# Kernel optimization log

Hardware: AMD Instinct MI355X
Metric: run time of the kernel (lower is better)

## Reference

```python
import jax, jax.numpy as jnp
import numpy as np

B, T, C, H = 64, 256, 384, 6
HS = C // H  # 64
EPS = 1e-3  # keras LayerNormalization default epsilon


def layernorm(x, gamma, beta):
    mu = jnp.mean(x, axis=-1, keepdims=True)
    var = jnp.var(x, axis=-1, keepdims=True)
    return (x - mu) * jax.lax.rsqrt(var + EPS) * gamma + beta


def setup_inputs() -> dict:
    key = jax.random.key(0)
    ks = jax.random.split(key, 12)
    s = lambda fan_in: 1.0 / np.sqrt(fan_in)
    return {
        "x": jax.random.normal(ks[0], (B, T, C), dtype=jnp.float32),
        "Wq": jax.random.normal(ks[1], (H, C, HS), dtype=jnp.float32) * s(C),
        "Wk": jax.random.normal(ks[2], (H, C, HS), dtype=jnp.float32) * s(C),
        "Wv": jax.random.normal(ks[3], (H, C, HS), dtype=jnp.float32) * s(C),
        "Wp": jax.random.normal(ks[4], (C, C), dtype=jnp.float32) * s(C),
        "bp": jnp.zeros((C,), dtype=jnp.float32),
        "W1": jax.random.normal(ks[5], (C, 4 * C), dtype=jnp.float32) * s(C),
        "b1": jnp.zeros((4 * C,), dtype=jnp.float32),
        "W2": jax.random.normal(ks[6], (4 * C, C), dtype=jnp.float32) * s(4 * C),
        "b2": jnp.zeros((C,), dtype=jnp.float32),
        "g1": jnp.ones((C,), dtype=jnp.float32),
        "be1": jnp.zeros((C,), dtype=jnp.float32),
        "g2": jnp.ones((C,), dtype=jnp.float32),
        "be2": jnp.zeros((C,), dtype=jnp.float32),
    }


def reference(x, Wq, Wk, Wv, Wp, bp, W1, b1, W2, b2, g1, be1, g2, be2):
    # --- self-attention sub-block (dropout is identity at inference) ---
    h = layernorm(x, g1, be1)                              # [B,T,C]
    q = jnp.einsum('btc,hcd->bhtd', h, Wq)                 # [B,H,T,HS]
    k = jnp.einsum('btc,hcd->bhtd', h, Wk)
    v = jnp.einsum('btc,hcd->bhtd', h, Wv)
    scale = HS ** -0.5
    wei = jnp.einsum('bhtd,bhsd->bhts', q, k) * scale      # [B,H,T,T]
    causal = jnp.tril(jnp.ones((T, T), dtype=bool))
    wei = jnp.where(causal[None, None], wei, -jnp.inf)
    att = jax.nn.softmax(wei, axis=-1)
    o = jnp.einsum('bhts,bhsd->bthd', att, v).reshape(B, T, C)  # concat heads
    sa = o @ Wp + bp
    x = x + sa
    # --- feed-forward sub-block ---
    h2 = layernorm(x, g2, be2)
    ff = jax.nn.relu(h2 @ W1 + b1) @ W2 + b2
    return x + ff
```

## Files before the change

### kernel.cpp

```cpp
#include <hip/hip_runtime.h>
#include <hip/hip_bf16.h>
#include <math.h>

#define Bn 64
#define Tn 256
#define Cn 384
#define Hn 6
#define HSn 64
#define FFn 1536
#define EPSn 1e-3f
#define SECn 6291456

typedef __attribute__((ext_vector_type(4))) float f32x4;
typedef __attribute__((ext_vector_type(2))) float f32x2;
typedef __attribute__((ext_vector_type(8))) short short8;
typedef __attribute__((ext_vector_type(4))) short short4v;
typedef __attribute__((ext_vector_type(2))) short short2v;

__device__ __forceinline__ short f2bf(float v) {
    __hip_bfloat16 h = __float2bfloat16(v);
    return *(short*)&h;
}


__global__ __launch_bounds__(256) void ln_pack_kernel(const float* __restrict__ x,
                                                      const float* __restrict__ g,
                                                      const float* __restrict__ be,
                                                      __hip_bfloat16* __restrict__ outPk) {
    int mt = blockIdx.x;
    int tid = threadIdx.x;
    int lane = tid & 63, wave = tid >> 6;
    __shared__ short rows[16 * 392];
#pragma unroll
    for (int i = 0; i < 4; i++) {
        int r = wave * 4 + i;
        const float* xr = x + ((size_t)mt * 16 + r) * Cn;
        f32x4 a = *(const f32x4*)(xr + lane * 4);
        f32x2 b = *(const f32x2*)(xr + 256 + lane * 2);
        float s = a.x + a.y + a.z + a.w + b.x + b.y;
#pragma unroll
        for (int off = 32; off; off >>= 1) s += __shfl_xor(s, off);
        float mu = s * (1.0f / Cn);
        f32x4 da = a - mu;
        f32x2 db = b - mu;
        float sq = da.x * da.x + da.y * da.y + da.z * da.z + da.w * da.w + db.x * db.x + db.y * db.y;
#pragma unroll
        for (int off = 32; off; off >>= 1) sq += __shfl_xor(sq, off);
        float rs = rsqrtf(sq * (1.0f / Cn) + EPSn);
        f32x4 g4 = *(const f32x4*)(g + lane * 4);
        f32x2 g2 = *(const f32x2*)(g + 256 + lane * 2);
        f32x4 e4 = *(const f32x4*)(be + lane * 4);
        f32x2 e2 = *(const f32x2*)(be + 256 + lane * 2);
        f32x4 y4 = da * rs * g4 + e4;
        f32x2 y2 = db * rs * g2 + e2;
        short4v o4 = {f2bf(y4.x), f2bf(y4.y), f2bf(y4.z), f2bf(y4.w)};
        *(short4v*)(&rows[r * 392 + lane * 4]) = o4;
        short2v o2 = {f2bf(y2.x), f2bf(y2.y)};
        *(short2v*)(&rows[r * 392 + 256 + lane * 2]) = o2;
    }
    __syncthreads();
    int r = lane & 15, q = lane >> 4;
#pragma unroll
    for (int p = 0; p < 3; p++) {
        int f = p * 4 + (tid >> 6);
        short8 v = *(const short8*)(&rows[r * 392 + f * 32 + q * 8]);
        *(short8*)((short*)outPk + ((size_t)mt * 12 + f) * 512 + lane * 8) = v;
    }
}

__global__ __launch_bounds__(256) void pack_b_kernel(const float* __restrict__ W,
                                                     __hip_bfloat16* __restrict__ out,
                                                     int K, int N) {
    int id = blockIdx.x * 256 + threadIdx.x;
    if (id >= K * N) return;
    int tile = id >> 9, lane = (id >> 3) & 63, j = id & 7;
    int ntiles = N >> 4;
    int k = (tile / ntiles) * 32 + ((lane >> 4) << 3) + j;
    int n = (tile % ntiles) * 16 + (lane & 15);
    out[id] = __float2bfloat16(W[(size_t)k * N + n]);
}

__global__ __launch_bounds__(256) void pack_qkv_kernel(const float* __restrict__ Wq,
                                                       const float* __restrict__ Wk,
                                                       const float* __restrict__ Wv,
                                                       __hip_bfloat16* __restrict__ out) {
    int id = blockIdx.x * 256 + threadIdx.x;
    if (id >= Cn * 1152) return;
    int tile = id >> 9, lane = (id >> 3) & 63, j = id & 7;
    int k = (tile / 72) * 32 + ((lane >> 4) << 3) + j;
    int n = (tile % 72) * 16 + (lane & 15);
    int sec = n / Cn, rem = n % Cn;
    int hh = rem >> 6, d = rem & 63;
    const float* W = (sec == 0) ? Wq : ((sec == 1) ? Wk : Wv);
    out[id] = __float2bfloat16(W[((size_t)hh * Cn + k) * HSn + d]);
}

template <int KK, int NN, int EPI>
__global__ __launch_bounds__(256) void gemm_mfma(const __hip_bfloat16* __restrict__ Apk,
                                                 const __hip_bfloat16* __restrict__ Bp,
                                                 const float* __restrict__ bias,
                                                 const float* __restrict__ resid,
                                                 float* __restrict__ outF,
                                                 __hip_bfloat16* __restrict__ outB) {
    constexpr int GX = NN / 64;
    constexpr int K32 = KK / 32;
    constexpr int NT16 = NN / 16;
    __shared__ __align__(16) char lds_raw[4 * 4864];

    int l = blockIdx.x;
    int xcd = l & 7, i = l >> 3;
    int rowblk = xcd * 16 + i / GX;
    int colblk = i - (i / GX) * GX;

    int lane = threadIdx.x & 63, wave = threadIdx.x >> 6;
    int lrow = lane & 15, lquad = lane >> 4;
    int m0 = rowblk * 128;
    int n0 = colblk * 64;
    int mt0 = (m0 >> 4) + wave * 2;

    f32x4 acc[2][4];
#pragma unroll
    for (int st = 0; st < 2; st++)
#pragma unroll
        for (int nt = 0; nt < 4; nt++) acc[st][nt] = (f32x4){0.f, 0.f, 0.f, 0.f};

    const short* a0p = (const short*)Apk + ((size_t)mt0 * K32) * 512 + lane * 8;
    const short* a1p = a0p + (size_t)K32 * 512;
    const short* bp0 = (const short*)Bp + ((size_t)(n0 >> 4)) * 512 + lane * 8;

#pragma unroll 6
    for (int kc = 0; kc < K32; kc++) {
        short8 af0 = *(const short8*)(a0p + (size_t)kc * 512);
        short8 af1 = *(const short8*)(a1p + (size_t)kc * 512);
#pragma unroll
        for (int nt = 0; nt < 4; nt++) {
            short8 bf = *(const short8*)(bp0 + ((size_t)kc * NT16 + nt) * 512);
            acc[0][nt] = __builtin_amdgcn_mfma_f32_16x16x32_bf16(af0, bf, acc[0][nt], 0, 0, 0);
            acc[1][nt] = __builtin_amdgcn_mfma_f32_16x16x32_bf16(af1, bf, acc[1][nt], 0, 0, 0);
        }
    }

    if (EPI == 1) {
        float* twf = (float*)(lds_raw + wave * 4864);
        float bnv[4];
#pragma unroll
        for (int nt = 0; nt < 4; nt++) bnv[nt] = bias[n0 + nt * 16 + lrow];
#pragma unroll
        for (int st = 0; st < 2; st++) {
            int mbase = m0 + (2 * wave + st) * 16;
#pragma unroll
            for (int nt = 0; nt < 4; nt++)
#pragma unroll
                for (int r = 0; r < 4; r++)
                    twf[(lquad * 4 + r) * 76 + nt * 16 + lrow] = acc[st][nt][r] + bnv[nt];
            int row = lane >> 2, seg = lane & 3;
            int m = mbase + row;
            const float* rrow = resid + (size_t)m * NN + n0 + seg * 16;
            float* orow = outF + (size_t)m * NN + n0 + seg * 16;
#pragma unroll
            for (int c = 0; c < 4; c++) {
                f32x4 vv = *(const f32x4*)(&twf[row * 76 + seg * 16 + c * 4]);
                f32x4 rv = *(const f32x4*)(rrow + c * 4);
                *(f32x4*)(orow + c * 4) = vv + rv;
            }
            __builtin_amdgcn_s_waitcnt(0);
        }
    } else {
        short* tws = (short*)(lds_raw + wave * 4864);
        float bnv[4];
        if (EPI == 2) {
#pragma unroll
            for (int nt = 0; nt < 4; nt++) bnv[nt] = bias[n0 + nt * 16 + lrow];
        }
#pragma unroll
        for (int st = 0; st < 2; st++)
#pragma unroll
            for (int nt = 0; nt < 4; nt++)
#pragma unroll
                for (int r = 0; r < 4; r++) {
                    float v = acc[st][nt][r];
                    if (EPI == 2) v = fmaxf(v + bnv[nt], 0.0f);
                    tws[(st * 16 + lquad * 4 + r) * 72 + nt * 16 + lrow] = f2bf(v);
                }
        if (EPI == 2) {
#pragma unroll
            for (int st2 = 0; st2 < 2; st2++) {
                int mt = (m0 >> 4) + wave * 2 + st2;
#pragma unroll
                for (int kcl = 0; kcl < 2; kcl++) {
                    int kc = (n0 >> 5) + kcl;
                    short8 v = *(const short8*)(
                        &tws[(st2 * 16 + (lane & 15)) * 72 + kcl * 32 + (lane >> 4) * 8]);
                    *(short8*)((short*)outB + ((size_t)mt * (NN / 32) + kc) * 512 + lane * 8) = v;
                }
            }
        } else {
            int sec = n0 / 384;
            int rem0 = n0 - sec * 384;
            int hh = rem0 >> 6;
            int b = m0 >> 8;
            int t_base = (m0 & 255) + wave * 32;
            int bh2 = b * Hn + hh;
            if (sec < 2) {
                short* outp = (short*)outB + (size_t)sec * SECn + (size_t)bh2 * 16384 +
                              (size_t)(t_base >> 4) * 1024 + lane * 8;
#pragma unroll
                for (int st2 = 0; st2 < 2; st2++)
#pragma unroll
                    for (int kc = 0; kc < 2; kc++) {
                        short8 v8 = *(const short8*)(
                            &tws[(st2 * 16 + (lane & 15)) * 72 + kc * 32 + (lane >> 4) * 8]);
                        *(short8*)(outp + (st2 * 2 + kc) * 512) = v8;
                    }
            } else {
                short* vout = (short*)outB + (size_t)2 * SECn + (size_t)bh2 * 16384 +
                              (size_t)((t_base >> 5) * 4) * 512;
#pragma unroll
                for (int dt = 0; dt < 4; dt++) {
                    short8 v8;
#pragma unroll
                    for (int j = 0; j < 8; j++) {
                        int t_loc = ((lane >> 4) << 3) + j;
                        v8[j] = tws[t_loc * 72 + dt * 16 + (lane & 15)];
                    }
                    *(short8*)(vout + dt * 512 + lane * 8) = v8;
                }
            }
        }
    }
}

__global__ __launch_bounds__(256) void attn_mfma_kernel(const __hip_bfloat16* __restrict__ qp,
                                                        const __hip_bfloat16* __restrict__ kp,
                                                        const __hip_bfloat16* __restrict__ vp,
                                                        __hip_bfloat16* __restrict__ o) {
    __shared__ short Pl[4 * 4096];
    int blk = blockIdx.x;
    int bh = blk % (Bn * Hn);
    int jg = blk / (Bn * Hn);
    int b = bh / Hn, hh = bh - b * Hn;
    int tid = threadIdx.x;
    int lane = tid & 63, wave = tid >> 6;
    int c16 = lane & 15, quad = lane >> 4;
    int qt = (wave << 2) + ((wave & 1) ? (3 - jg) : jg);

    const short* qs = (const short*)qp + (size_t)bh * 16384 + (size_t)qt * 1024 + lane * 8;
    const short* ks = (const short*)kp + (size_t)bh * 16384 + lane * 8;
    const short* vs = (const short*)vp + (size_t)bh * 16384 + lane * 8;
    short* Pw = Pl + wave * 4096;

    short8 aq0 = *(const short8*)(qs);
    short8 aq1 = *(const short8*)(qs + 512);

    int st_max = qt;
    int kb_count = (qt + 2) >> 1;
    int covered = kb_count * 2;
    int qrow0 = qt * 16;

    f32x4 accS[16];
#pragma unroll
    for (int st = 0; st < 16; st++) accS[st] = (f32x4){0.f, 0.f, 0.f, 0.f};
#pragma unroll
    for (int st = 0; st < 16; st++) {
        if (st <= st_max) {
            short8 bk0 = *(const short8*)(ks + st * 1024);
            short8 bk1 = *(const short8*)(ks + st * 1024 + 512);
            accS[st] = __builtin_amdgcn_mfma_f32_16x16x32_bf16(aq0, bk0, accS[st], 0, 0, 0);
            accS[st] = __builtin_amdgcn_mfma_f32_16x16x32_bf16(aq1, bk1, accS[st], 0, 0, 0);
        }
    }

    float inv[4];
#pragma unroll
    for (int r = 0; r < 4; r++) {
        int row = qrow0 + quad * 4 + r;
        float mx = -INFINITY;
#pragma unroll
        for (int st = 0; st < 16; st++) {
            if (st <= st_max) {
                int col = st * 16 + c16;
                float a = (col <= row) ? accS[st][r] * 0.125f : -INFINITY;
                accS[st][r] = a;
                mx = fmaxf(mx, a);
            }
        }
#pragma unroll
        for (int off = 8; off; off >>= 1) mx = fmaxf(mx, __shfl_xor(mx, off));
        float sum = 0.f;
#pragma unroll
        for (int st = 0; st < 16; st++) {
            if (st < covered) {
                float e = 0.0f;
                if (st <= st_max) {
                    e = __expf(accS[st][r] - mx);
                    sum += e;
                }
                int c = st * 16 + c16;
                Pw[(c >> 5) * 512 + (((c >> 3) & 3) * 16 + quad * 4 + r) * 8 + (c & 7)] =
                    f2bf(e);
            }
        }
#pragma unroll
        for (int off = 8; off; off >>= 1) sum += __shfl_xor(sum, off);
        inv[r] = 1.0f / sum;
    }

    f32x4 accO[4];
#pragma unroll
    for (int nt = 0; nt < 4; nt++) accO[nt] = (f32x4){0.f, 0.f, 0.f, 0.f};
#pragma unroll
    for (int kbi = 0; kbi < 8; kbi++) {
        if (kbi < kb_count) {
            short8 ap = *(const short8*)(Pw + kbi * 512 + lane * 8);
#pragma unroll
            for (int nt = 0; nt < 4; nt++) {
                short8 bv = *(const short8*)(vs + (kbi * 4 + nt) * 512);
                accO[nt] = __builtin_amdgcn_mfma_f32_16x16x32_bf16(ap, bv, accO[nt], 0, 0, 0);
            }
        }
    }

#pragma unroll
    for (int nt = 0; nt < 4; nt++)
#pragma unroll
        for (int r = 0; r < 4; r++)
            Pw[(quad * 4 + r) * 72 + nt * 16 + c16] = f2bf(accO[nt][r] * inv[r]);
    int mt = (b << 4) + qt;
#pragma unroll
    for (int kcl = 0; kcl < 2; kcl++) {
        short8 v = *(const short8*)(&Pw[(lane & 15) * 72 + kcl * 32 + (lane >> 4) * 8]);
        *(short8*)((short*)o + ((size_t)mt * 12 + hh * 2 + kcl) * 512 + lane * 8) = v;
    }
}

extern "C" void kernel_launch(void* const* d_in, const int* in_sizes, int n_in,
                              void* d_out, int out_size, void* d_ws, size_t ws_size,
                              hipStream_t stream) {
    const float* x  = (const float*)d_in[0];
    const float* Wq = (const float*)d_in[1];
    const float* Wk = (const float*)d_in[2];
    const float* Wv = (const float*)d_in[3];
    const float* Wp = (const float*)d_in[4];
    const float* bp = (const float*)d_in[5];
    const float* W1 = (const float*)d_in[6];
    const float* b1 = (const float*)d_in[7];
    const float* W2 = (const float*)d_in[8];
    const float* b2 = (const float*)d_in[9];
    const float* g1 = (const float*)d_in[10];
    const float* be1 = (const float*)d_in[11];
    const float* g2 = (const float*)d_in[12];
    const float* be2 = (const float*)d_in[13];

    const size_t M = (size_t)Bn * Tn;
    __hip_bfloat16* ws  = (__hip_bfloat16*)d_ws;
    __hip_bfloat16* h   = ws;
    __hip_bfloat16* big = h + M * Cn;
    __hip_bfloat16* o   = big + M * FFn;
    __hip_bfloat16* pQKV = o + M * Cn;
    __hip_bfloat16* pWp  = pQKV + Cn * 1152;
    __hip_bfloat16* pW1  = pWp + Cn * Cn;
    __hip_bfloat16* pW2  = pW1 + Cn * FFn;

    float* x2 = (float*)d_out;

    pack_qkv_kernel<<<(Cn * 1152 + 255) / 256, 256, 0, stream>>>(Wq, Wk, Wv, pQKV);
    pack_b_kernel<<<(Cn * Cn + 255) / 256, 256, 0, stream>>>(Wp, pWp, Cn, Cn);
    pack_b_kernel<<<(Cn * FFn + 255) / 256, 256, 0, stream>>>(W1, pW1, Cn, FFn);
    pack_b_kernel<<<(FFn * Cn + 255) / 256, 256, 0, stream>>>(W2, pW2, FFn, Cn);

    ln_pack_kernel<<<M / 16, 256, 0, stream>>>(x, g1, be1, h);
    gemm_mfma<Cn, 1152, 0><<<2304, 256, 0, stream>>>(h, pQKV, nullptr, nullptr, nullptr, big);
    attn_mfma_kernel<<<Bn * Hn * 4, 256, 0, stream>>>(big, big + SECn, big + 2 * SECn, o);
    gemm_mfma<Cn, Cn, 1><<<768, 256, 0, stream>>>(o, pWp, bp, x, x2, nullptr);
    ln_pack_kernel<<<M / 16, 256, 0, stream>>>(x2, g2, be2, h);
    gemm_mfma<Cn, FFn, 2><<<3072, 256, 0, stream>>>(h, pW1, b1, nullptr, nullptr, big);
    gemm_mfma<FFn, Cn, 1><<<768, 256, 0, stream>>>(big, pW2, b2, x2, x2, nullptr);
}
```

Measured before the change: 267.4 us.

## Stage B tiles in LDS via async global_load_lds with double buffering

```diff
diff --git a/kernel.cpp b/kernel.cpp
--- a/kernel.cpp
+++ b/kernel.cpp
@@ -16,6 +16,12 @@
 typedef __attribute__((ext_vector_type(8))) short short8;
 typedef __attribute__((ext_vector_type(4))) short short4v;
 typedef __attribute__((ext_vector_type(2))) short short2v;
+
+__device__ __forceinline__ void async_copy16(void* lds, const void* g) {
+    __builtin_amdgcn_global_load_lds(
+        (const __attribute__((address_space(1))) void*)g,
+        (__attribute__((address_space(3))) void*)lds, 16, 0, 0);
+}
 
 __device__ __forceinline__ short f2bf(float v) {
     __hip_bfloat16 h = __float2bfloat16(v);
@@ -104,8 +110,9 @@
                                                  __hip_bfloat16* __restrict__ outB) {
     constexpr int GX = NN / 64;
     constexpr int K32 = KK / 32;
+    constexpr int NC = K32 / 4;
     constexpr int NT16 = NN / 16;
-    __shared__ __align__(16) char lds_raw[4 * 4864];
+    __shared__ __align__(16) short ldsB[2 * 8192];
 
     int l = blockIdx.x;
     int xcd = l & 7, i = l >> 3;
@@ -126,22 +133,49 @@
 
     const short* a0p = (const short*)Apk + ((size_t)mt0 * K32) * 512 + lane * 8;
     const short* a1p = a0p + (size_t)K32 * 512;
-    const short* bp0 = (const short*)Bp + ((size_t)(n0 >> 4)) * 512 + lane * 8;
-
-#pragma unroll 6
-    for (int kc = 0; kc < K32; kc++) {
-        short8 af0 = *(const short8*)(a0p + (size_t)kc * 512);
-        short8 af1 = *(const short8*)(a1p + (size_t)kc * 512);
-#pragma unroll
-        for (int nt = 0; nt < 4; nt++) {
-            short8 bf = *(const short8*)(bp0 + ((size_t)kc * NT16 + nt) * 512);
-            acc[0][nt] = __builtin_amdgcn_mfma_f32_16x16x32_bf16(af0, bf, acc[0][nt], 0, 0, 0);
-            acc[1][nt] = __builtin_amdgcn_mfma_f32_16x16x32_bf16(af1, bf, acc[1][nt], 0, 0, 0);
-        }
-    }
+    const short* bsrc = (const short*)Bp + ((size_t)wave * NT16 + (n0 >> 4)) * 512 + lane * 8;
+    short* bdst0 = ldsB + wave * 2048;
+
+#pragma unroll
+    for (int nt = 0; nt < 4; nt++) async_copy16(bdst0 + nt * 512, bsrc + nt * 512);
+    short8 aR[2][2][4];
+#pragma unroll
+    for (int kf = 0; kf < 4; kf++) {
+        aR[0][0][kf] = *(const short8*)(a0p + kf * 512);
+        aR[0][1][kf] = *(const short8*)(a1p + kf * 512);
+    }
+
+#pragma unroll
+    for (int c = 0; c < NC; c++) {
+        __syncthreads();
+        if (c + 1 < NC) {
+            const short* bs = bsrc + (size_t)(c + 1) * 4 * NT16 * 512;
+            short* bd = ldsB + ((c + 1) & 1) * 8192 + wave * 2048;
+#pragma unroll
+            for (int nt = 0; nt < 4; nt++) async_copy16(bd + nt * 512, bs + nt * 512);
+#pragma unroll
+            for (int kf = 0; kf < 4; kf++) {
+                aR[(c + 1) & 1][0][kf] = *(const short8*)(a0p + ((c + 1) * 4 + kf) * 512);
+                aR[(c + 1) & 1][1][kf] = *(const short8*)(a1p + ((c + 1) * 4 + kf) * 512);
+            }
+        }
+        const short* bl = ldsB + (c & 1) * 8192 + lane * 8;
+#pragma unroll
+        for (int kf = 0; kf < 4; kf++) {
+#pragma unroll
+            for (int nt = 0; nt < 4; nt++) {
+                short8 bf = *(const short8*)(bl + (kf * 4 + nt) * 512);
+                acc[0][nt] = __builtin_amdgcn_mfma_f32_16x16x32_bf16(aR[c & 1][0][kf], bf,
+                                                                     acc[0][nt], 0, 0, 0);
+                acc[1][nt] = __builtin_amdgcn_mfma_f32_16x16x32_bf16(aR[c & 1][1][kf], bf,
+                                                                     acc[1][nt], 0, 0, 0);
+            }
+        }
+    }
+    __syncthreads();
 
     if (EPI == 1) {
-        float* twf = (float*)(lds_raw + wave * 4864);
+        float* twf = (float*)((char*)ldsB + wave * 4864);
         float bnv[4];
 #pragma unroll
         for (int nt = 0; nt < 4; nt++) bnv[nt] = bias[n0 + nt * 16 + lrow];
@@ -166,7 +200,7 @@
             __builtin_amdgcn_s_waitcnt(0);
         }
     } else {
-        short* tws = (short*)(lds_raw + wave * 4864);
+        short* tws = (short*)((char*)ldsB + wave * 4864);
         float bnv[4];
         if (EPI == 2) {
 #pragma unroll
```

Measured after the change: 236.9 us. -11.4%, faster.
